# Performance work log

Measured on AMD Instinct MI355X. Metric: run time of the kernel, lower is better.

The kernel has to match this reference:

```python
import jax, jax.numpy as jnp
import numpy as np

B, N, H, E, D = 8, 2048, 1024, 8, 2048


def setup_inputs() -> dict:
    key = jax.random.key(0)
    k = jax.random.split(key, 5)
    x = jax.random.normal(k[0], (B, N, H), dtype=jnp.float32)
    Wr = jax.random.normal(k[1], (H, E), dtype=jnp.float32) * 0.02
    br = jnp.zeros((E,), dtype=jnp.float32)
    W1 = jax.random.normal(k[2], (E, H, D), dtype=jnp.float32) * 0.02
    b1 = jnp.zeros((E, D), dtype=jnp.float32)
    W2 = jax.random.normal(k[3], (E, D, H), dtype=jnp.float32) * 0.02
    b2 = jnp.zeros((E, H), dtype=jnp.float32)
    return {"x": x, "Wr": Wr, "br": br, "W1": W1, "b1": b1, "W2": W2, "b2": b2}


def reference(x, Wr, br, W1, b1, W2, b2):
    # x: [B,N,H]; router v1, top-1, eval mode (no expert dropout)
    Bx, Nx, Hx = x.shape
    Ex = Wr.shape[1]
    x_flat = x.reshape(Bx * Nx, Hx)                      # [T,H]
    logits = x_flat @ Wr + br                            # [T,E]
    probs = jax.nn.softmax(logits, axis=-1)              # [T,E]
    expert_idx = jnp.argmax(probs, axis=-1)              # [T]

    out_flat = jnp.zeros_like(x_flat)
    for e in range(Ex):  # small fixed loop over experts
        h = jax.nn.gelu(x_flat @ W1[e] + b1[e], approximate=False)  # exact erf GELU (torch default)
        eout = h @ W2[e] + b2[e]                         # [T,H]
        out_flat = jnp.where((expert_idx == e)[:, None], eout, out_flat)

    out = x + out_flat.reshape(Bx, Nx, Hx)               # residual

    p_i = probs.mean(axis=0)                             # [E]
    balance_loss = Ex * jnp.sum(p_i ** 2)
    EPS = 1e-8
    entropy = -jnp.sum(probs * jnp.log(probs + EPS), axis=-1)
    entropy_loss = entropy.mean()
    tokens_per_expert = jnp.bincount(expert_idx, length=Ex)
    return out, balance_loss, entropy_loss, tokens_per_expert
```

## Files before the change

### kernel.cpp

```cpp
#include <hip/hip_runtime.h>
#include <math.h>

#define TT 16384
#define HH 1024
#define DD 2048
#define EE 8
#define MAXTILES 160

typedef float f32x4 __attribute__((ext_vector_type(4)));
typedef __bf16 bf16x8 __attribute__((ext_vector_type(8)));

__device__ __forceinline__ unsigned short f2bf(float f) {
  union { float f; unsigned u; } v; v.f = f;
  unsigned r = v.u + 0x7FFFu + ((v.u >> 16) & 1u);
  return (unsigned short)(r >> 16);
}

__device__ __forceinline__ void gl2lds16(const unsigned short* g, unsigned short* l) {
  __builtin_amdgcn_global_load_lds(
      (const __attribute__((address_space(1))) void*)g,
      (__attribute__((address_space(3))) void*)l, 16, 0, 0);
}

__global__ __launch_bounds__(256) void k_transpose2(const float* __restrict__ W1s,
                                                    unsigned short* __restrict__ W1d,
                                                    const float* __restrict__ W2s,
                                                    unsigned short* __restrict__ W2d,
                                                    int* counts, float* probs_sum,
                                                    float* ent_sum, int* ticket) {
  if (blockIdx.x == 0) {
    int t0 = threadIdx.x;
    if (t0 < EE) { counts[t0] = 0; probs_sum[t0] = 0.f; }
    if (t0 == 0) { *ent_sum = 0.f; *ticket = 0; }
  }
  const int T1 = EE * (HH / 64) * (DD / 64);
  int bid = blockIdx.x;
  const float* src; unsigned short* dst; int R, C;
  if (bid < T1) { src = W1s; dst = W1d; R = HH; C = DD; }
  else          { bid -= T1; src = W2s; dst = W2d; R = DD; C = HH; }
  int tilesC = C >> 6, tilesR = R >> 6;
  int e = bid / (tilesR * tilesC);
  int rem = bid % (tilesR * tilesC);
  int tr = rem / tilesC, tc = rem % tilesC;
  const float* s = src + (size_t)e * R * C + (size_t)(tr * 64) * C + tc * 64;
  unsigned short* d = dst + (size_t)e * R * C + (size_t)(tc * 64) * R + tr * 64;

  __shared__ float t2[64][65];
  int t = threadIdx.x;
  int col = t & 63, rbase = t >> 6;
#pragma unroll
  for (int i = 0; i < 16; ++i) {
    int row = rbase + i * 4;
    t2[col][row] = s[(size_t)row * C + col];
  }
  __syncthreads();
#pragma unroll
  for (int i = 0; i < 4; ++i) {
    int p = t + i * 256;
    int rr = p >> 4, ch = (p & 15) << 2;
    ushort4 o;
    o.x = f2bf(t2[rr][ch + 0]);
    o.y = f2bf(t2[rr][ch + 1]);
    o.z = f2bf(t2[rr][ch + 2]);
    o.w = f2bf(t2[rr][ch + 3]);
    *(ushort4*)&d[(size_t)rr * R + ch] = o;
  }
}

__global__ __launch_bounds__(256) void k_router(const float* __restrict__ x,
                                                const float* __restrict__ Wr,
                                                const float* __restrict__ br,
                                                int* __restrict__ eidx,
                                                float* __restrict__ probs_sum,
                                                float* __restrict__ ent_sum,
                                                int* __restrict__ counts,
                                                unsigned short* __restrict__ xb,
                                                int* __restrict__ ticket,
                                                int* __restrict__ offsets,
                                                int* __restrict__ cursor,
                                                int* __restrict__ tileE,
                                                int* __restrict__ tileR0,
                                                int* __restrict__ tileEnd,
                                                int* __restrict__ nTiles,
                                                float* __restrict__ out_scalars) {
  __shared__ float s_p[EE];
  __shared__ int   s_c[EE];
  __shared__ float s_e;
  __shared__ int   s_last;
  int tid = threadIdx.x;
  if (tid < EE) { s_p[tid] = 0.f; s_c[tid] = 0; }
  if (tid == 0) s_e = 0.f;
  __syncthreads();
  int lane = tid & 63, w = tid >> 6;
  for (int tt = 0; tt < 4; ++tt) {
    int token = blockIdx.x * 16 + w * 4 + tt;
    double acc[EE];
#pragma unroll
    for (int e = 0; e < EE; ++e) acc[e] = 0.0;
    const float* xr = x + (size_t)token * HH;
    unsigned short* xo = xb + (size_t)token * HH;
#pragma unroll
    for (int i = 0; i < 4; ++i) {
      int hh = i * 256 + lane * 4;
      f32x4 xf = *(const f32x4*)&xr[hh];
      ushort4 o;
      o.x = f2bf(xf[0]); o.y = f2bf(xf[1]); o.z = f2bf(xf[2]); o.w = f2bf(xf[3]);
      *(ushort4*)&xo[hh] = o;
#pragma unroll
      for (int k = 0; k < 4; ++k) {
        double xv = (double)xf[k];
        const float* wr = Wr + (size_t)(hh + k) * EE;
#pragma unroll
        for (int e = 0; e < EE; ++e) acc[e] += xv * (double)wr[e];
      }
    }
#pragma unroll
    for (int off = 32; off > 0; off >>= 1) {
#pragma unroll
      for (int e = 0; e < EE; ++e) acc[e] += __shfl_down(acc[e], off);
    }
    if (lane == 0) {
      double l[EE];
#pragma unroll
      for (int e = 0; e < EE; ++e) l[e] = acc[e] + (double)br[e];
      double m = l[0]; int am = 0;
#pragma unroll
      for (int e = 1; e < EE; ++e) { if (l[e] > m) { m = l[e]; am = e; } }
      float p[EE]; float s = 0.f;
#pragma unroll
      for (int e = 0; e < EE; ++e) { p[e] = __expf((float)(l[e] - m)); s += p[e]; }
      float inv = 1.0f / s; float ent = 0.f;
#pragma unroll
      for (int e = 0; e < EE; ++e) { p[e] *= inv; ent -= p[e] * __logf(p[e] + 1e-8f); }
      eidx[token] = am;
#pragma unroll
      for (int e = 0; e < EE; ++e) atomicAdd(&s_p[e], p[e]);
      atomicAdd(&s_e, ent);
      atomicAdd(&s_c[am], 1);
    }
  }
  __syncthreads();
  if (tid < EE) { atomicAdd(&probs_sum[tid], s_p[tid]); atomicAdd(&counts[tid], s_c[tid]); }
  if (tid == 0) atomicAdd(ent_sum, s_e);
  if (tid == 0) {
    __threadfence();
    int done = atomicAdd(ticket, 1);
    s_last = (done == (int)gridDim.x - 1) ? 1 : 0;
  }
  __syncthreads();
  if (s_last) {
    __shared__ int soff[EE + 1];
    __shared__ int tbase[EE + 1];
    __shared__ int scnt[EE];
    if (tid == 0) {
      int off = 0, tb = 0; float bal = 0.f;
      for (int e = 0; e < EE; ++e) {
        int c = atomicAdd(&counts[e], 0);
        float ps = atomicAdd(&probs_sum[e], 0.f);
        scnt[e] = c; soff[e] = off; offsets[e] = off; cursor[e] = off;
        tbase[e] = tb;
        tb += (c + 127) >> 7;
        off += c;
        float pi = ps / (float)TT; bal += pi * pi;
        out_scalars[2 + e] = (float)c;
      }
      soff[EE] = off; offsets[EE] = off; tbase[EE] = tb;
      *nTiles = tb;
      out_scalars[0] = (float)EE * bal;
      out_scalars[1] = atomicAdd(ent_sum, 0.f) / (float)TT;
    }
    __syncthreads();
    int nt = tbase[EE];
    for (int i = tid; i < nt; i += 256) {
      int e = 0;
      while (tbase[e + 1] <= i) ++e;
      int j = i - tbase[e];
      tileE[i] = e; tileR0[i] = soff[e] + j * 128; tileEnd[i] = soff[e] + scnt[e];
    }
  }
}

__global__ __launch_bounds__(256) void k_perm(const int* __restrict__ eidx,
                                              int* cursor, int* __restrict__ perm) {
  int t = blockIdx.x * 256 + threadIdx.x;
  int lane = threadIdx.x & 63;
  int mye = eidx[t];
  int pos = 0;
#pragma unroll
  for (int e = 0; e < EE; ++e) {
    unsigned long long mask = __ballot(mye == e);
    if (mask == 0ull) continue;
    int leader = __ffsll(mask) - 1;
    int base = 0;
    if (lane == leader) base = atomicAdd(&cursor[e], __popcll(mask));
    base = __shfl(base, leader);
    if (mye == e) pos = base + (int)__popcll(mask & ((1ull << lane) - 1ull));
  }
  perm[pos] = t;
}


__global__ __launch_bounds__(256) void k_gemm1(const unsigned short* __restrict__ xb,
                                               const unsigned short* __restrict__ Wt1,
                                               const float* __restrict__ b1,
                                               const int* __restrict__ perm,
                                               const int* __restrict__ tileE,
                                               const int* __restrict__ tileR0,
                                               const int* __restrict__ tileEnd,
                                               const int* __restrict__ nTiles,
                                               unsigned short* __restrict__ hbuf) {
  int tile = blockIdx.y;
  if (tile >= *nTiles) return;
  int e = tileE[tile], r0 = tileR0[tile], rend = tileEnd[tile];
  int c0 = blockIdx.x * 128;
  __shared__ __align__(16) unsigned short As[128 * 64];
  __shared__ __align__(16) unsigned short Bs[128 * 64];
  int tid = threadIdx.x, lane = tid & 63, w = tid >> 6;
  int wr = w >> 1, wc = w & 1;
  int quad = lane >> 4, l16 = lane & 15;
  int lrow = lane >> 3, lslot = lane & 7;
  int sslot = lslot ^ lrow;
  const unsigned short* aP[4];
  const unsigned short* bP[4];
  unsigned short* aL[4];
  unsigned short* bL[4];
  const unsigned short* bBase = Wt1 + (size_t)e * ((size_t)DD * HH);
#pragma unroll
  for (int i = 0; i < 4; ++i) {
    int ar = w * 32 + i * 8 + lrow;
    int g = r0 + ar; if (g >= rend) g = rend - 1;
    aP[i] = xb + (size_t)perm[g] * HH + sslot * 8;
    bP[i] = bBase + (size_t)(c0 + ar) * HH + sslot * 8;
    aL[i] = &As[(w * 32 + i * 8) * 64];
    bL[i] = &Bs[(w * 32 + i * 8) * 64];
  }
  f32x4 acc[4][4] = {};
  for (int k0 = 0; k0 < HH; k0 += 64) {
#pragma unroll
    for (int i = 0; i < 4; ++i) { gl2lds16(aP[i] + k0, aL[i]); gl2lds16(bP[i] + k0, bL[i]); }
    __syncthreads();
#pragma unroll
    for (int h = 0; h < 2; ++h) {
      bf16x8 a[4], b[4];
#pragma unroll
      for (int i = 0; i < 4; ++i)
        a[i] = *(const bf16x8*)&As[(wr * 64 + i * 16 + l16) * 64 + (((h << 2) | quad) ^ (l16 & 7)) * 8];
#pragma unroll
      for (int j = 0; j < 4; ++j)
        b[j] = *(const bf16x8*)&Bs[(wc * 64 + j * 16 + l16) * 64 + (((h << 2) | quad) ^ (l16 & 7)) * 8];
#pragma unroll
      for (int i = 0; i < 4; ++i)
#pragma unroll
        for (int j = 0; j < 4; ++j)
          acc[i][j] = __builtin_amdgcn_mfma_f32_16x16x32_bf16(a[i], b[j], acc[i][j], 0, 0, 0);
    }
    __syncthreads();
  }
  float bias[4];
#pragma unroll
  for (int j = 0; j < 4; ++j) bias[j] = b1[e * DD + c0 + wc * 64 + j * 16 + l16];
#pragma unroll
  for (int i = 0; i < 4; ++i) {
#pragma unroll
    for (int r = 0; r < 4; ++r) {
      int gr = r0 + wr * 64 + i * 16 + quad * 4 + r;
      if (gr < rend) {
#pragma unroll
        for (int j = 0; j < 4; ++j) {
          int col = c0 + wc * 64 + j * 16 + l16;
          float v = acc[i][j][r] + bias[j];
          v = 0.5f * v * (1.0f + erff(v * 0.70710678118654752f));
          hbuf[(size_t)gr * DD + col] = f2bf(v);
        }
      }
    }
  }
}

__global__ __launch_bounds__(256) void k_gemm2(const unsigned short* __restrict__ hbuf,
                                               const unsigned short* __restrict__ Wt2,
                                               const float* __restrict__ b2,
                                               const float* __restrict__ x,
                                               const int* __restrict__ perm,
                                               const int* __restrict__ tileE,
                                               const int* __restrict__ tileR0,
                                               const int* __restrict__ tileEnd,
                                               const int* __restrict__ nTiles,
                                               float* __restrict__ outp) {
  int tile = blockIdx.y;
  if (tile >= *nTiles) return;
  int e = tileE[tile], r0 = tileR0[tile], rend = tileEnd[tile];
  int c0 = blockIdx.x * 128;
  __shared__ __align__(16) unsigned short As[128 * 64];
  __shared__ __align__(16) unsigned short Bs[128 * 64];
  int tid = threadIdx.x, lane = tid & 63, w = tid >> 6;
  int wr = w >> 1, wc = w & 1;
  int quad = lane >> 4, l16 = lane & 15;
  int lrow = lane >> 3, lslot = lane & 7;
  int sslot = lslot ^ lrow;
  const unsigned short* aP[4];
  const unsigned short* bP[4];
  unsigned short* aL[4];
  unsigned short* bL[4];
  const unsigned short* bBase = Wt2 + (size_t)e * ((size_t)HH * DD);
#pragma unroll
  for (int i = 0; i < 4; ++i) {
    int ar = w * 32 + i * 8 + lrow;
    int g = r0 + ar; if (g >= rend) g = rend - 1;
    aP[i] = hbuf + (size_t)g * DD + sslot * 8;
    bP[i] = bBase + (size_t)(c0 + ar) * DD + sslot * 8;
    aL[i] = &As[(w * 32 + i * 8) * 64];
    bL[i] = &Bs[(w * 32 + i * 8) * 64];
  }
  f32x4 acc[4][4] = {};
  for (int k0 = 0; k0 < DD; k0 += 64) {
#pragma unroll
    for (int i = 0; i < 4; ++i) { gl2lds16(aP[i] + k0, aL[i]); gl2lds16(bP[i] + k0, bL[i]); }
    __syncthreads();
#pragma unroll
    for (int h = 0; h < 2; ++h) {
      bf16x8 a[4], b[4];
#pragma unroll
      for (int i = 0; i < 4; ++i)
        a[i] = *(const bf16x8*)&As[(wr * 64 + i * 16 + l16) * 64 + (((h << 2) | quad) ^ (l16 & 7)) * 8];
#pragma unroll
      for (int j = 0; j < 4; ++j)
        b[j] = *(const bf16x8*)&Bs[(wc * 64 + j * 16 + l16) * 64 + (((h << 2) | quad) ^ (l16 & 7)) * 8];
#pragma unroll
      for (int i = 0; i < 4; ++i)
#pragma unroll
        for (int j = 0; j < 4; ++j)
          acc[i][j] = __builtin_amdgcn_mfma_f32_16x16x32_bf16(a[i], b[j], acc[i][j], 0, 0, 0);
    }
    __syncthreads();
  }
  float bias[4];
#pragma unroll
  for (int j = 0; j < 4; ++j) bias[j] = b2[e * HH + c0 + wc * 64 + j * 16 + l16];
#pragma unroll
  for (int i = 0; i < 4; ++i) {
#pragma unroll
    for (int r = 0; r < 4; ++r) {
      int gr = r0 + wr * 64 + i * 16 + quad * 4 + r;
      if (gr < rend) {
        int tok = perm[gr];
#pragma unroll
        for (int j = 0; j < 4; ++j) {
          int col = c0 + wc * 64 + j * 16 + l16;
          size_t oi = (size_t)tok * HH + col;
          outp[oi] = x[oi] + bias[j] + acc[i][j][r];
        }
      }
    }
  }
}

extern "C" void kernel_launch(void* const* d_in, const int* in_sizes, int n_in,
                              void* d_out, int out_size, void* d_ws, size_t ws_size,
                              hipStream_t stream) {
  const float* x  = (const float*)d_in[0];
  const float* Wr = (const float*)d_in[1];
  const float* br = (const float*)d_in[2];
  const float* W1 = (const float*)d_in[3];
  const float* b1 = (const float*)d_in[4];
  const float* W2 = (const float*)d_in[5];
  const float* b2 = (const float*)d_in[6];
  float* outp = (float*)d_out;

  char* ws = (char*)d_ws;
  int*   counts    = (int*)(ws + 0);
  int*   cursor    = (int*)(ws + 64);
  int*   nTiles    = (int*)(ws + 128);
  float* probs_sum = (float*)(ws + 192);
  float* ent_sum   = (float*)(ws + 256);
  int*   offsets   = (int*)(ws + 320);
  int*   ticket    = (int*)(ws + 448);
  int*   tileE     = (int*)(ws + 512);
  int*   tileR0    = (int*)(ws + 2048);
  int*   tileEnd   = (int*)(ws + 3584);
  int*   eidx      = (int*)(ws + 8192);
  int*   perm      = (int*)(ws + 8192 + 4 * (size_t)TT);
  size_t off = 8192 + 8 * (size_t)TT;
  unsigned short* xb   = (unsigned short*)(ws + off); off += (size_t)TT * HH * 2;
  unsigned short* Wt1  = (unsigned short*)(ws + off); off += (size_t)EE * DD * HH * 2;
  unsigned short* Wt2  = (unsigned short*)(ws + off); off += (size_t)EE * HH * DD * 2;
  unsigned short* hbuf = (unsigned short*)(ws + off); off += (size_t)TT * DD * 2;

  float* out_scalars = outp + (size_t)TT * HH;

  k_transpose2<<<2 * EE * (HH / 64) * (DD / 64), 256, 0, stream>>>(
      W1, Wt1, W2, Wt2, counts, probs_sum, ent_sum, ticket);
  k_router<<<TT / 16, 256, 0, stream>>>(x, Wr, br, eidx, probs_sum, ent_sum, counts, xb,
                                        ticket, offsets, cursor, tileE, tileR0, tileEnd,
                                        nTiles, out_scalars);
  k_perm<<<TT / 256, 256, 0, stream>>>(eidx, cursor, perm);
  dim3 g1(DD / 128, MAXTILES);
  k_gemm1<<<g1, 256, 0, stream>>>(xb, Wt1, b1, perm, tileE, tileR0, tileEnd, nTiles, hbuf);
  dim3 g2(HH / 128, MAXTILES);
  k_gemm2<<<g2, 256, 0, stream>>>(hbuf, Wt2, b2, x, perm, tileE, tileR0, tileEnd, nTiles, outp);
}
```

Baseline: 616.7 us.

## Widen expert GEMM tiles to 128x256 with 32-deep K steps

Both expert GEMM kernels move from 128x128 output tiles with a 64-wide K step to 128x256 tiles with a 32-wide K step. Each wave now accumulates a 4x8 grid of MFMA fragments, and the column-block count in the launch grid is halved. The aim is more reuse of each loaded A row across output columns and less redundant traffic for the gathered activations. In exchange, the XOR swizzle on the LDS layout is dropped, which risks LDS bank conflicts. The shallower K step doubles the number of barriers per K, and the smaller grid may leave compute units underused.

```diff
diff --git a/kernel.cpp b/kernel.cpp
--- a/kernel.cpp
+++ b/kernel.cpp
@@ -212,53 +212,51 @@
   int tile = blockIdx.y;
   if (tile >= *nTiles) return;
   int e = tileE[tile], r0 = tileR0[tile], rend = tileEnd[tile];
-  int c0 = blockIdx.x * 128;
-  __shared__ __align__(16) unsigned short As[128 * 64];
-  __shared__ __align__(16) unsigned short Bs[128 * 64];
+  int c0 = blockIdx.x * 256;
+  __shared__ __align__(16) unsigned short As[128 * 32];
+  __shared__ __align__(16) unsigned short Bs[256 * 32];
   int tid = threadIdx.x, lane = tid & 63, w = tid >> 6;
   int wr = w >> 1, wc = w & 1;
   int quad = lane >> 4, l16 = lane & 15;
-  int lrow = lane >> 3, lslot = lane & 7;
-  int sslot = lslot ^ lrow;
-  const unsigned short* aP[4];
-  const unsigned short* bP[4];
-  unsigned short* aL[4];
+  int srow = lane >> 2, seg = lane & 3;
+  int g0 = r0 + w * 32 + srow;      if (g0 >= rend) g0 = rend - 1;
+  int g1 = r0 + w * 32 + 16 + srow; if (g1 >= rend) g1 = rend - 1;
+  const unsigned short* aG0 = xb + (size_t)perm[g0] * HH + seg * 8;
+  const unsigned short* aG1 = xb + (size_t)perm[g1] * HH + seg * 8;
+  const unsigned short* bBase = Wt1 + (size_t)e * ((size_t)DD * HH);
+  const unsigned short* bG[4];
   unsigned short* bL[4];
-  const unsigned short* bBase = Wt1 + (size_t)e * ((size_t)DD * HH);
-#pragma unroll
-  for (int i = 0; i < 4; ++i) {
-    int ar = w * 32 + i * 8 + lrow;
-    int g = r0 + ar; if (g >= rend) g = rend - 1;
-    aP[i] = xb + (size_t)perm[g] * HH + sslot * 8;
-    bP[i] = bBase + (size_t)(c0 + ar) * HH + sslot * 8;
-    aL[i] = &As[(w * 32 + i * 8) * 64];
-    bL[i] = &Bs[(w * 32 + i * 8) * 64];
-  }
-  f32x4 acc[4][4] = {};
-  for (int k0 = 0; k0 < HH; k0 += 64) {
-#pragma unroll
-    for (int i = 0; i < 4; ++i) { gl2lds16(aP[i] + k0, aL[i]); gl2lds16(bP[i] + k0, bL[i]); }
-    __syncthreads();
-#pragma unroll
-    for (int h = 0; h < 2; ++h) {
-      bf16x8 a[4], b[4];
-#pragma unroll
-      for (int i = 0; i < 4; ++i)
-        a[i] = *(const bf16x8*)&As[(wr * 64 + i * 16 + l16) * 64 + (((h << 2) | quad) ^ (l16 & 7)) * 8];
-#pragma unroll
-      for (int j = 0; j < 4; ++j)
-        b[j] = *(const bf16x8*)&Bs[(wc * 64 + j * 16 + l16) * 64 + (((h << 2) | quad) ^ (l16 & 7)) * 8];
-#pragma unroll
-      for (int i = 0; i < 4; ++i)
-#pragma unroll
-        for (int j = 0; j < 4; ++j)
-          acc[i][j] = __builtin_amdgcn_mfma_f32_16x16x32_bf16(a[i], b[j], acc[i][j], 0, 0, 0);
-    }
-    __syncthreads();
-  }
-  float bias[4];
-#pragma unroll
-  for (int j = 0; j < 4; ++j) bias[j] = b1[e * DD + c0 + wc * 64 + j * 16 + l16];
+#pragma unroll
+  for (int k = 0; k < 4; ++k) {
+    bG[k] = bBase + (size_t)(c0 + w * 64 + k * 16 + srow) * HH + seg * 8;
+    bL[k] = &Bs[(w * 64 + k * 16) * 32];
+  }
+  unsigned short* aL0 = &As[(w * 32 + 0) * 32];
+  unsigned short* aL1 = &As[(w * 32 + 16) * 32];
+  f32x4 acc[4][8] = {};
+  for (int k0 = 0; k0 < HH; k0 += 32) {
+    gl2lds16(aG0 + k0, aL0);
+    gl2lds16(aG1 + k0, aL1);
+#pragma unroll
+    for (int k = 0; k < 4; ++k) gl2lds16(bG[k] + k0, bL[k]);
+    __syncthreads();
+    bf16x8 a[4], b[8];
+#pragma unroll
+    for (int i = 0; i < 4; ++i)
+      a[i] = *(const bf16x8*)&As[(wr * 64 + i * 16 + l16) * 32 + quad * 8];
+#pragma unroll
+    for (int j = 0; j < 8; ++j)
+      b[j] = *(const bf16x8*)&Bs[(wc * 128 + j * 16 + l16) * 32 + quad * 8];
+#pragma unroll
+    for (int i = 0; i < 4; ++i)
+#pragma unroll
+      for (int j = 0; j < 8; ++j)
+        acc[i][j] = __builtin_amdgcn_mfma_f32_16x16x32_bf16(a[i], b[j], acc[i][j], 0, 0, 0);
+    __syncthreads();
+  }
+  float bias[8];
+#pragma unroll
+  for (int j = 0; j < 8; ++j) bias[j] = b1[e * DD + c0 + wc * 128 + j * 16 + l16];
 #pragma unroll
   for (int i = 0; i < 4; ++i) {
 #pragma unroll
@@ -266,8 +264,8 @@
       int gr = r0 + wr * 64 + i * 16 + quad * 4 + r;
       if (gr < rend) {
 #pragma unroll
-        for (int j = 0; j < 4; ++j) {
-          int col = c0 + wc * 64 + j * 16 + l16;
+        for (int j = 0; j < 8; ++j) {
+          int col = c0 + wc * 128 + j * 16 + l16;
           float v = acc[i][j][r] + bias[j];
           v = 0.5f * v * (1.0f + erff(v * 0.70710678118654752f));
           hbuf[(size_t)gr * DD + col] = f2bf(v);
@@ -290,53 +288,51 @@
   int tile = blockIdx.y;
   if (tile >= *nTiles) return;
   int e = tileE[tile], r0 = tileR0[tile], rend = tileEnd[tile];
-  int c0 = blockIdx.x * 128;
-  __shared__ __align__(16) unsigned short As[128 * 64];
-  __shared__ __align__(16) unsigned short Bs[128 * 64];
+  int c0 = blockIdx.x * 256;
+  __shared__ __align__(16) unsigned short As[128 * 32];
+  __shared__ __align__(16) unsigned short Bs[256 * 32];
   int tid = threadIdx.x, lane = tid & 63, w = tid >> 6;
   int wr = w >> 1, wc = w & 1;
   int quad = lane >> 4, l16 = lane & 15;
-  int lrow = lane >> 3, lslot = lane & 7;
-  int sslot = lslot ^ lrow;
-  const unsigned short* aP[4];
-  const unsigned short* bP[4];
-  unsigned short* aL[4];
+  int srow = lane >> 2, seg = lane & 3;
+  int g0 = r0 + w * 32 + srow;      if (g0 >= rend) g0 = rend - 1;
+  int g1 = r0 + w * 32 + 16 + srow; if (g1 >= rend) g1 = rend - 1;
+  const unsigned short* aG0 = hbuf + (size_t)g0 * DD + seg * 8;
+  const unsigned short* aG1 = hbuf + (size_t)g1 * DD + seg * 8;
+  const unsigned short* bBase = Wt2 + (size_t)e * ((size_t)HH * DD);
+  const unsigned short* bG[4];
   unsigned short* bL[4];
-  const unsigned short* bBase = Wt2 + (size_t)e * ((size_t)HH * DD);
-#pragma unroll
-  for (int i = 0; i < 4; ++i) {
-    int ar = w * 32 + i * 8 + lrow;
-    int g = r0 + ar; if (g >= rend) g = rend - 1;
-    aP[i] = hbuf + (size_t)g * DD + sslot * 8;
-    bP[i] = bBase + (size_t)(c0 + ar) * DD + sslot * 8;
-    aL[i] = &As[(w * 32 + i * 8) * 64];
-    bL[i] = &Bs[(w * 32 + i * 8) * 64];
-  }
-  f32x4 acc[4][4] = {};
-  for (int k0 = 0; k0 < DD; k0 += 64) {
-#pragma unroll
-    for (int i = 0; i < 4; ++i) { gl2lds16(aP[i] + k0, aL[i]); gl2lds16(bP[i] + k0, bL[i]); }
-    __syncthreads();
-#pragma unroll
-    for (int h = 0; h < 2; ++h) {
-      bf16x8 a[4], b[4];
-#pragma unroll
-      for (int i = 0; i < 4; ++i)
-        a[i] = *(const bf16x8*)&As[(wr * 64 + i * 16 + l16) * 64 + (((h << 2) | quad) ^ (l16 & 7)) * 8];
-#pragma unroll
-      for (int j = 0; j < 4; ++j)
-        b[j] = *(const bf16x8*)&Bs[(wc * 64 + j * 16 + l16) * 64 + (((h << 2) | quad) ^ (l16 & 7)) * 8];
-#pragma unroll
-      for (int i = 0; i < 4; ++i)
-#pragma unroll
-        for (int j = 0; j < 4; ++j)
-          acc[i][j] = __builtin_amdgcn_mfma_f32_16x16x32_bf16(a[i], b[j], acc[i][j], 0, 0, 0);
-    }
-    __syncthreads();
-  }
-  float bias[4];
-#pragma unroll
-  for (int j = 0; j < 4; ++j) bias[j] = b2[e * HH + c0 + wc * 64 + j * 16 + l16];
+#pragma unroll
+  for (int k = 0; k < 4; ++k) {
+    bG[k] = bBase + (size_t)(c0 + w * 64 + k * 16 + srow) * DD + seg * 8;
+    bL[k] = &Bs[(w * 64 + k * 16) * 32];
+  }
+  unsigned short* aL0 = &As[(w * 32 + 0) * 32];
+  unsigned short* aL1 = &As[(w * 32 + 16) * 32];
+  f32x4 acc[4][8] = {};
+  for (int k0 = 0; k0 < DD; k0 += 32) {
+    gl2lds16(aG0 + k0, aL0);
+    gl2lds16(aG1 + k0, aL1);
+#pragma unroll
+    for (int k = 0; k < 4; ++k) gl2lds16(bG[k] + k0, bL[k]);
+    __syncthreads();
+    bf16x8 a[4], b[8];
+#pragma unroll
+    for (int i = 0; i < 4; ++i)
+      a[i] = *(const bf16x8*)&As[(wr * 64 + i * 16 + l16) * 32 + quad * 8];
+#pragma unroll
+    for (int j = 0; j < 8; ++j)
+      b[j] = *(const bf16x8*)&Bs[(wc * 128 + j * 16 + l16) * 32 + quad * 8];
+#pragma unroll
+    for (int i = 0; i < 4; ++i)
+#pragma unroll
+      for (int j = 0; j < 8; ++j)
+        acc[i][j] = __builtin_amdgcn_mfma_f32_16x16x32_bf16(a[i], b[j], acc[i][j], 0, 0, 0);
+    __syncthreads();
+  }
+  float bias[8];
+#pragma unroll
+  for (int j = 0; j < 8; ++j) bias[j] = b2[e * HH + c0 + wc * 128 + j * 16 + l16];
 #pragma unroll
   for (int i = 0; i < 4; ++i) {
 #pragma unroll
@@ -345,8 +341,8 @@
       if (gr < rend) {
         int tok = perm[gr];
 #pragma unroll
-        for (int j = 0; j < 4; ++j) {
-          int col = c0 + wc * 64 + j * 16 + l16;
+        for (int j = 0; j < 8; ++j) {
+          int col = c0 + wc * 128 + j * 16 + l16;
           size_t oi = (size_t)tok * HH + col;
           outp[oi] = x[oi] + bias[j] + acc[i][j][r];
         }
@@ -394,8 +390,8 @@
                                         ticket, offsets, cursor, tileE, tileR0, tileEnd,
                                         nTiles, out_scalars);
   k_perm<<<TT / 256, 256, 0, stream>>>(eidx, cursor, perm);
-  dim3 g1(DD / 128, MAXTILES);
+  dim3 g1(DD / 256, MAXTILES);
   k_gemm1<<<g1, 256, 0, stream>>>(xb, Wt1, b1, perm, tileE, tileR0, tileEnd, nTiles, hbuf);
-  dim3 g2(HH / 128, MAXTILES);
+  dim3 g2(HH / 256, MAXTILES);
   k_gemm2<<<g2, 256, 0, stream>>>(hbuf, Wt2, b2, x, perm, tileE, tileR0, tileEnd, nTiles, outp);
 }
```

New measurement: 800.4 us. 29.8% more time.

## Double-buffer LDS tiles in both expert GEMMs to overlap loads with MFMA

Applied to the files above, without the earlier changes.

Both grouped GEMM kernels now split each 64-wide K step into two 32-wide stages held in two separate LDS buffers. The global-to-LDS copy of the next stage is issued before the MFMAs on the current stage, so memory latency can overlap with compute instead of stalling at each barrier. The tiles are now 32 elements wide with no XOR swizzle, and the load mapping changes to 4 lanes per row. This keeps the same barrier count per 64 elements of K. The risk is that barrier-induced waits still serialize part of the copy, and that the narrower stages give less work per synchronization.

```diff
diff --git a/kernel.cpp b/kernel.cpp
--- a/kernel.cpp
+++ b/kernel.cpp
@@ -200,6 +200,27 @@
 }
 
 
+#define GEMM_COMPUTE(AS, BS)                                                   \
+  {                                                                            \
+    bf16x8 a[4], b[4];                                                         \
+    _Pragma("unroll") for (int i = 0; i < 4; ++i)                              \
+        a[i] = *(const bf16x8*)&AS[(wr * 64 + i * 16 + l16) * 32 + quad * 8];  \
+    _Pragma("unroll") for (int j = 0; j < 4; ++j)                              \
+        b[j] = *(const bf16x8*)&BS[(wc * 64 + j * 16 + l16) * 32 + quad * 8];  \
+    _Pragma("unroll") for (int i = 0; i < 4; ++i)                              \
+        _Pragma("unroll") for (int j = 0; j < 4; ++j)                          \
+            acc[i][j] = __builtin_amdgcn_mfma_f32_16x16x32_bf16(               \
+                a[i], b[j], acc[i][j], 0, 0, 0);                               \
+  }
+
+#define GEMM_STAGE(AS, BS, KOFF)                                               \
+  {                                                                            \
+    gl2lds16(aG0 + (KOFF), AS + base0);                                        \
+    gl2lds16(aG1 + (KOFF), AS + base1);                                        \
+    gl2lds16(bG0 + (KOFF), BS + base0);                                        \
+    gl2lds16(bG1 + (KOFF), BS + base1);                                        \
+  }
+
 __global__ __launch_bounds__(256) void k_gemm1(const unsigned short* __restrict__ xb,
                                                const unsigned short* __restrict__ Wt1,
                                                const float* __restrict__ b1,
@@ -213,48 +234,32 @@
   if (tile >= *nTiles) return;
   int e = tileE[tile], r0 = tileR0[tile], rend = tileEnd[tile];
   int c0 = blockIdx.x * 128;
-  __shared__ __align__(16) unsigned short As[128 * 64];
-  __shared__ __align__(16) unsigned short Bs[128 * 64];
+  __shared__ __align__(16) unsigned short As0[128 * 32];
+  __shared__ __align__(16) unsigned short Bs0[128 * 32];
+  __shared__ __align__(16) unsigned short As1[128 * 32];
+  __shared__ __align__(16) unsigned short Bs1[128 * 32];
   int tid = threadIdx.x, lane = tid & 63, w = tid >> 6;
   int wr = w >> 1, wc = w & 1;
   int quad = lane >> 4, l16 = lane & 15;
-  int lrow = lane >> 3, lslot = lane & 7;
-  int sslot = lslot ^ lrow;
-  const unsigned short* aP[4];
-  const unsigned short* bP[4];
-  unsigned short* aL[4];
-  unsigned short* bL[4];
+  int srow = lane >> 2, seg = lane & 3;
+  int ar0 = w * 32 + srow, ar1 = ar0 + 16;
+  int g0 = r0 + ar0; if (g0 >= rend) g0 = rend - 1;
+  int g1 = r0 + ar1; if (g1 >= rend) g1 = rend - 1;
+  const unsigned short* aG0 = xb + (size_t)perm[g0] * HH + seg * 8;
+  const unsigned short* aG1 = xb + (size_t)perm[g1] * HH + seg * 8;
   const unsigned short* bBase = Wt1 + (size_t)e * ((size_t)DD * HH);
-#pragma unroll
-  for (int i = 0; i < 4; ++i) {
-    int ar = w * 32 + i * 8 + lrow;
-    int g = r0 + ar; if (g >= rend) g = rend - 1;
-    aP[i] = xb + (size_t)perm[g] * HH + sslot * 8;
-    bP[i] = bBase + (size_t)(c0 + ar) * HH + sslot * 8;
-    aL[i] = &As[(w * 32 + i * 8) * 64];
-    bL[i] = &Bs[(w * 32 + i * 8) * 64];
-  }
+  const unsigned short* bG0 = bBase + (size_t)(c0 + ar0) * HH + seg * 8;
+  const unsigned short* bG1 = bBase + (size_t)(c0 + ar1) * HH + seg * 8;
+  const int base0 = (w * 32 + 0) * 32, base1 = (w * 32 + 16) * 32;
   f32x4 acc[4][4] = {};
+  GEMM_STAGE(As0, Bs0, 0);
   for (int k0 = 0; k0 < HH; k0 += 64) {
-#pragma unroll
-    for (int i = 0; i < 4; ++i) { gl2lds16(aP[i] + k0, aL[i]); gl2lds16(bP[i] + k0, bL[i]); }
-    __syncthreads();
-#pragma unroll
-    for (int h = 0; h < 2; ++h) {
-      bf16x8 a[4], b[4];
-#pragma unroll
-      for (int i = 0; i < 4; ++i)
-        a[i] = *(const bf16x8*)&As[(wr * 64 + i * 16 + l16) * 64 + (((h << 2) | quad) ^ (l16 & 7)) * 8];
-#pragma unroll
-      for (int j = 0; j < 4; ++j)
-        b[j] = *(const bf16x8*)&Bs[(wc * 64 + j * 16 + l16) * 64 + (((h << 2) | quad) ^ (l16 & 7)) * 8];
-#pragma unroll
-      for (int i = 0; i < 4; ++i)
-#pragma unroll
-        for (int j = 0; j < 4; ++j)
-          acc[i][j] = __builtin_amdgcn_mfma_f32_16x16x32_bf16(a[i], b[j], acc[i][j], 0, 0, 0);
-    }
-    __syncthreads();
+    __syncthreads();
+    if (k0 + 32 < HH) GEMM_STAGE(As1, Bs1, k0 + 32);
+    GEMM_COMPUTE(As0, Bs0);
+    __syncthreads();
+    if (k0 + 64 < HH) GEMM_STAGE(As0, Bs0, k0 + 64);
+    GEMM_COMPUTE(As1, Bs1);
   }
   float bias[4];
 #pragma unroll
@@ -291,48 +296,32 @@
   if (tile >= *nTiles) return;
   int e = tileE[tile], r0 = tileR0[tile], rend = tileEnd[tile];
   int c0 = blockIdx.x * 128;
-  __shared__ __align__(16) unsigned short As[128 * 64];
-  __shared__ __align__(16) unsigned short Bs[128 * 64];
+  __shared__ __align__(16) unsigned short As0[128 * 32];
+  __shared__ __align__(16) unsigned short Bs0[128 * 32];
+  __shared__ __align__(16) unsigned short As1[128 * 32];
+  __shared__ __align__(16) unsigned short Bs1[128 * 32];
   int tid = threadIdx.x, lane = tid & 63, w = tid >> 6;
   int wr = w >> 1, wc = w & 1;
   int quad = lane >> 4, l16 = lane & 15;
-  int lrow = lane >> 3, lslot = lane & 7;
-  int sslot = lslot ^ lrow;
-  const unsigned short* aP[4];
-  const unsigned short* bP[4];
-  unsigned short* aL[4];
-  unsigned short* bL[4];
+  int srow = lane >> 2, seg = lane & 3;
+  int ar0 = w * 32 + srow, ar1 = ar0 + 16;
+  int g0 = r0 + ar0; if (g0 >= rend) g0 = rend - 1;
+  int g1 = r0 + ar1; if (g1 >= rend) g1 = rend - 1;
+  const unsigned short* aG0 = hbuf + (size_t)g0 * DD + seg * 8;
+  const unsigned short* aG1 = hbuf + (size_t)g1 * DD + seg * 8;
   const unsigned short* bBase = Wt2 + (size_t)e * ((size_t)HH * DD);
-#pragma unroll
-  for (int i = 0; i < 4; ++i) {
-    int ar = w * 32 + i * 8 + lrow;
-    int g = r0 + ar; if (g >= rend) g = rend - 1;
-    aP[i] = hbuf + (size_t)g * DD + sslot * 8;
-    bP[i] = bBase + (size_t)(c0 + ar) * DD + sslot * 8;
-    aL[i] = &As[(w * 32 + i * 8) * 64];
-    bL[i] = &Bs[(w * 32 + i * 8) * 64];
-  }
+  const unsigned short* bG0 = bBase + (size_t)(c0 + ar0) * DD + seg * 8;
+  const unsigned short* bG1 = bBase + (size_t)(c0 + ar1) * DD + seg * 8;
+  const int base0 = (w * 32 + 0) * 32, base1 = (w * 32 + 16) * 32;
   f32x4 acc[4][4] = {};
+  GEMM_STAGE(As0, Bs0, 0);
   for (int k0 = 0; k0 < DD; k0 += 64) {
-#pragma unroll
-    for (int i = 0; i < 4; ++i) { gl2lds16(aP[i] + k0, aL[i]); gl2lds16(bP[i] + k0, bL[i]); }
-    __syncthreads();
-#pragma unroll
-    for (int h = 0; h < 2; ++h) {
-      bf16x8 a[4], b[4];
-#pragma unroll
-      for (int i = 0; i < 4; ++i)
-        a[i] = *(const bf16x8*)&As[(wr * 64 + i * 16 + l16) * 64 + (((h << 2) | quad) ^ (l16 & 7)) * 8];
-#pragma unroll
-      for (int j = 0; j < 4; ++j)
-        b[j] = *(const bf16x8*)&Bs[(wc * 64 + j * 16 + l16) * 64 + (((h << 2) | quad) ^ (l16 & 7)) * 8];
-#pragma unroll
-      for (int i = 0; i < 4; ++i)
-#pragma unroll
-        for (int j = 0; j < 4; ++j)
-          acc[i][j] = __builtin_amdgcn_mfma_f32_16x16x32_bf16(a[i], b[j], acc[i][j], 0, 0, 0);
-    }
-    __syncthreads();
+    __syncthreads();
+    if (k0 + 32 < DD) GEMM_STAGE(As1, Bs1, k0 + 32);
+    GEMM_COMPUTE(As0, Bs0);
+    __syncthreads();
+    if (k0 + 64 < DD) GEMM_STAGE(As0, Bs0, k0 + 64);
+    GEMM_COMPUTE(As1, Bs1);
   }
   float bias[4];
 #pragma unroll
```

New measurement: 585.2 us. 1.05x faster.
